# Optimization experiments

Hardware: AMD Instinct MI355X
Metric: run time of the kernel (lower is better)

The kernel has to match this reference:

```python
import jax, jax.numpy as jnp
import numpy as np

D_MODEL = 1024
NUM_MODULES = 8
MAX_TRANSLATION = 3.0
MAX_ROT_ANGLE = 3.141592653589793


def setup_inputs() -> dict:
    key = jax.random.key(0)
    k1, k2, k3, k4 = jax.random.split(key, 4)
    B, N = 8, 8192
    node_feats = jax.random.normal(k1, (B, N, D_MODEL), jnp.float32)
    coords = jax.random.normal(k2, (B, N, 3), jnp.float32)
    W = jax.random.normal(k3, (NUM_MODULES * 8, D_MODEL), jnp.float32) * (1.0 / np.sqrt(D_MODEL))
    b = jax.random.normal(k4, (NUM_MODULES * 8,), jnp.float32) * 0.01
    return {"node_feats": node_feats, "coords": coords, "W": W, "b": b}


def _normalize(x, eps=1e-12):
    return x / jnp.clip(jnp.linalg.norm(x, axis=-1, keepdims=True), eps)


def _axis_angle_to_quaternion(aa):
    # pytorch3d convention: quat = [cos(theta/2), axis * sin(theta/2)]
    angles = jnp.linalg.norm(aa, axis=-1, keepdims=True)
    half = angles * 0.5
    small = jnp.abs(angles) < 1e-6
    safe_angles = jnp.where(small, 1.0, angles)
    sin_half_over_angle = jnp.where(small, 0.5 - angles * angles / 48.0, jnp.sin(half) / safe_angles)
    return jnp.concatenate([jnp.cos(half), aa * sin_half_over_angle], axis=-1)


def _quat_mul(a, b):
    aw, ax, ay, az = a[..., 0], a[..., 1], a[..., 2], a[..., 3]
    bw, bx, by, bz = b[..., 0], b[..., 1], b[..., 2], b[..., 3]
    ow = aw * bw - ax * bx - ay * by - az * bz
    ox = aw * bx + ax * bw + ay * bz - az * by
    oy = aw * by - ax * bz + ay * bw + az * bx
    oz = aw * bz + ax * by - ay * bx + az * bw
    return jnp.stack([ow, ox, oy, oz], axis=-1)


def _quat_apply(q, p):
    # q: [B,1,4], p: [B,N,3] -> rotate points: im(q * (0,p) * q^-1)
    pq = jnp.concatenate([jnp.zeros_like(p[..., :1]), p], axis=-1)
    q_inv = q * jnp.array([1.0, -1.0, -1.0, -1.0], q.dtype)
    return _quat_mul(_quat_mul(q, pq), q_inv)[..., 1:]


def reference(node_feats, coords, W, b):
    B, N, _ = coords.shape
    params = (node_feats @ W.T + b).reshape(B, N, NUM_MODULES, 8)
    anchor_logits = params[..., 0:1]   # [B,N,M,1]
    select_logits = params[..., 1:2]
    rot_axis = params[..., 2:5]
    trans = params[..., 5:8]

    anchor_w = jax.nn.softmax(anchor_logits, axis=1)      # softmax over N
    select_p = jax.nn.sigmoid(select_logits)

    angles = jnp.linalg.norm(rot_axis, axis=-1, keepdims=True)
    axis_n = _normalize(rot_axis)
    angles = jnp.tanh(angles) * MAX_ROT_ANGLE
    quats = _axis_angle_to_quaternion(axis_n * angles)    # [B,N,M,4]
    trans = jnp.tanh(trans) * MAX_TRANSLATION             # [B,N,M,3]

    xs = (jnp.moveaxis(quats, 2, 0),     # [M,B,N,4]
          jnp.moveaxis(trans, 2, 0),     # [M,B,N,3]
          jnp.moveaxis(anchor_w, 2, 0),  # [M,B,N,1]
          jnp.moveaxis(select_p, 2, 0))  # [M,B,N,1]

    def step(c, per):
        q, t, aw, sp = per
        anchor = jnp.sum(c * aw, axis=1, keepdims=True)               # [B,1,3]
        s = jnp.clip(jnp.sum(sp, axis=1, keepdims=True), 1e-8)        # [B,1,1]
        q_group = _normalize(jnp.sum(q * sp, axis=1, keepdims=True) / s)  # [B,1,4]
        t_group = jnp.sum(t * sp, axis=1, keepdims=True) / s          # [B,1,3]
        moved = _quat_apply(q_group, c - anchor) + anchor + t_group   # [B,N,3]
        return c + sp * (moved - c), None                             # lerp

    out, _ = jax.lax.scan(step, coords, xs)
    return out
```

## Files before the change

### kernel.cpp

```cpp
#include <hip/hip_runtime.h>
#include <hip/hip_bf16.h>
#include <hip/hip_fp16.h>
#include <math.h>

#define D_MODEL 1024
#define NMOD 8
#define BATCH 8
#define NNODE 8192
#define PI_F 3.14159265358979323846f
#define MAXT 3.0f

typedef short bf16x8 __attribute__((ext_vector_type(8)));
typedef float f32x4 __attribute__((ext_vector_type(4)));

__device__ inline unsigned short f2bf(float x) {
    __hip_bfloat16 h = __float2bfloat16(x);
    return __builtin_bit_cast(unsigned short, h);
}
__device__ inline float h2f(unsigned short u) {
    __half h = __builtin_bit_cast(__half, u);
    return __half2float(h);
}
__device__ inline unsigned short f2h(float x) {
    __half h = __float2half(x);
    return __builtin_bit_cast(unsigned short, h);
}

__global__ void pack_b(const float* __restrict__ W, unsigned short* __restrict__ Bpk,
                       float* __restrict__ sums) {
    int t = blockIdx.x * 256 + threadIdx.x;
    if (t < BATCH * NMOD * 8) sums[t] = 0.f;
    int l  = t & 63;
    int g  = (t >> 6) & 3;
    int ks = t >> 8;
    int j  = g * 16 + (l & 15);
    int k0 = ks * 32 + ((l >> 4) * 8);
    const float* wp = &W[(size_t)j * D_MODEL + k0];
    bf16x8 pack;
    #pragma unroll
    for (int r = 0; r < 8; ++r) pack[r] = (short)f2bf(wp[r]);
    *reinterpret_cast<bf16x8*>(Bpk + (size_t)t * 8) = pack;
}

__device__ __forceinline__ void loadg2(float4 (&dst)[4], const float* arow, int g) {
    #pragma unroll
    for (int i = 0; i < 2; ++i) {
        dst[2 * i]     = *reinterpret_cast<const float4*>(arow + (g * 2 + i) * 32);
        dst[2 * i + 1] = *reinterpret_cast<const float4*>(arow + (g * 2 + i) * 32 + 4);
    }
}

__device__ __forceinline__ void compg2(const float4 (&src)[4], int g,
                                       const unsigned short* __restrict__ Blds, int lane,
                                       f32x4 (&acc)[4]) {
    #pragma unroll
    for (int i = 0; i < 2; ++i) {
        float f[8] = {src[2*i].x, src[2*i].y, src[2*i].z, src[2*i].w,
                      src[2*i+1].x, src[2*i+1].y, src[2*i+1].z, src[2*i+1].w};
        bf16x8 a;
        #pragma unroll
        for (int j = 0; j < 8; ++j) a[j] = (short)f2bf(f[j]);
        const int ks = g * 2 + i;
        #pragma unroll
        for (int gg = 0; gg < 4; ++gg) {
            bf16x8 bh = *reinterpret_cast<const bf16x8*>(
                Blds + ((size_t)((ks * 4 + gg) * 64 + lane)) * 8);
            acc[gg] = __builtin_amdgcn_mfma_f32_16x16x32_bf16(a, bh, acc[gg], 0, 0, 0);
        }
    }
}

__global__ __launch_bounds__(1024) void gemm_mfma(
    const float* __restrict__ feats, const unsigned short* __restrict__ Bpk,
    const float* __restrict__ bias,
    unsigned int* __restrict__ esp_out,
    float* __restrict__ sums)
{
    __shared__ __align__(16) unsigned char smem[131072];

    const int tid  = threadIdx.x;
    const int lane = tid & 63;
    const int wv   = tid >> 6;

    {
        const char* gsrc = (const char*)Bpk;
        #pragma unroll
        for (int r = 0; r < 8; ++r) {
            const int off = r * 16384 + wv * 1024;
            __builtin_amdgcn_global_load_lds(
                (const __attribute__((address_space(1))) unsigned int*)(gsrc + off + lane * 16),
                (__attribute__((address_space(3))) unsigned int*)(smem + off),
                16, 0, 0);
        }
    }

    const int mt    = blockIdx.x * 16 + wv;
    const int mbase = mt * 16;
    const float* arow = feats + (size_t)(mbase + (lane & 15)) * D_MODEL + ((lane >> 4) * 8);
    const unsigned short* Blds = (const unsigned short*)smem;

    f32x4 acc[4];
    #pragma unroll
    for (int g = 0; g < 4; ++g) acc[g] = (f32x4){0.f, 0.f, 0.f, 0.f};

    float4 Ab[4][4];
    #pragma unroll
    for (int i = 0; i < 4; ++i) loadg2(Ab[i], arow, i);

    __syncthreads();

    #pragma unroll
    for (int i = 0; i < 16; ++i) {
        compg2(Ab[i & 3], i, Blds, lane, acc);
        if (i + 4 < 16) loadg2(Ab[i & 3], arow, i + 4);
    }

    __syncthreads();
    float* pbuf = reinterpret_cast<float*>(smem) + (size_t)wv * (16 * 68);
    float* sacc = reinterpret_cast<float*>(smem + 69632);
    if (tid < 64) sacc[tid] = 0.f;

    #pragma unroll
    for (int g = 0; g < 4; ++g) {
        float bj = bias[g * 16 + (lane & 15)];
        #pragma unroll
        for (int r = 0; r < 4; ++r)
            pbuf[((lane >> 4) * 4 + r) * 68 + g * 16 + (lane & 15)] = acc[g][r] + bj;
    }
    __syncthreads();

    const int b    = mbase >> 13;
    const int nInB = mbase & 8191;

    #pragma unroll
    for (int h = 0; h < 2; ++h) {
        const int node = lane & 15;
        const int m    = (lane >> 4) + 4 * h;
        const float* pa = &pbuf[node * 68 + m * 8];
        float al = pa[0], sl = pa[1];
        float ax = pa[2], ay = pa[3], az = pa[4];
        float tx = pa[5], ty = pa[6], tz = pa[7];

        float ew = expf(al);
        float sp = 1.f / (1.f + expf(-sl));

        float n0  = sqrtf(ax * ax + ay * ay + az * az);
        float inv = 1.f / fmaxf(n0, 1e-12f);
        float ang = tanhf(n0) * PI_F;
        float hf  = 0.5f * ang;
        float shoa = (ang < 1e-6f) ? (0.5f - ang * ang * (1.f / 48.f))
                                   : (sinf(hf) / ang);
        float qw = cosf(hf);
        float fac = inv * ang * shoa;
        float qx = ax * fac, qy = ay * fac, qz = az * fac;

        float ttx = tanhf(tx) * MAXT, tty = tanhf(ty) * MAXT, ttz = tanhf(tz) * MAXT;

        size_t base = ((size_t)(b * NMOD + m)) * NNODE + nInB + node;
        esp_out[base] = ((unsigned)f2h(sp) << 16) | (unsigned)f2h(ew);

        float red[8];
        red[0] = sp;
        red[1] = sp * qw; red[2] = sp * qx; red[3] = sp * qy; red[4] = sp * qz;
        red[5] = sp * ttx; red[6] = sp * tty; red[7] = sp * ttz;
        #pragma unroll
        for (int v = 0; v < 8; ++v) {
            #pragma unroll
            for (int o = 1; o < 16; o <<= 1) red[v] += __shfl_xor(red[v], o);
        }
        if ((lane & 15) == 0) {
            #pragma unroll
            for (int v = 0; v < 8; ++v) atomicAdd(&sacc[m * 8 + v], red[v]);
        }
    }
    __syncthreads();
    if (tid < 64) atomicAdd(&sums[b * 64 + tid], sacc[tid]);
}

__global__ __launch_bounds__(1024) void scan_coords(
    const float* __restrict__ coords,
    const unsigned int* __restrict__ esp_in,
    const float* __restrict__ sums, float* __restrict__ out)
{
    const int b   = blockIdx.x;
    const int tid = threadIdx.x;
    const int lane = tid & 63, wid = tid >> 6;
    __shared__ float redbuf[64];
    __shared__ float bcast[4];

    const int n0 = tid * 8;

    float cx[8], cy[8], cz[8];
    {
        float c[24];
        const float4* cp4 = reinterpret_cast<const float4*>(
            &coords[((size_t)b * NNODE + n0) * 3]);
        #pragma unroll
        for (int q = 0; q < 6; ++q) {
            float4 v = cp4[q];
            c[q * 4 + 0] = v.x; c[q * 4 + 1] = v.y;
            c[q * 4 + 2] = v.z; c[q * 4 + 3] = v.w;
        }
        #pragma unroll
        for (int i = 0; i < 8; ++i) { cx[i] = c[3*i]; cy[i] = c[3*i+1]; cz[i] = c[3*i+2]; }
    }

    const uint4* esp4 = reinterpret_cast<const uint4*>(
        &esp_in[(size_t)b * NMOD * NNODE]);
    uint4 cur0 = esp4[(0 * NNODE + n0) >> 2];
    uint4 cur1 = esp4[((0 * NNODE + n0) >> 2) + 1];

    for (int m = 0; m < NMOD; ++m) {
        const int mn = (m + 1 < NMOD) ? m + 1 : m;
        uint4 nxt0 = esp4[(mn * NNODE + n0) >> 2];
        uint4 nxt1 = esp4[((mn * NNODE + n0) >> 2) + 1];

        unsigned pk[8] = {cur0.x, cur0.y, cur0.z, cur0.w, cur1.x, cur1.y, cur1.z, cur1.w};
        float ev[8], spl[8];
        #pragma unroll
        for (int i = 0; i < 8; ++i) {
            ev[i]  = h2f((unsigned short)(pk[i] & 0xFFFFu));
            spl[i] = h2f((unsigned short)(pk[i] >> 16));
        }

        float se = 0.f, sx = 0.f, sy = 0.f, sz = 0.f;
        #pragma unroll
        for (int i = 0; i < 8; ++i) {
            se += ev[i]; sx += ev[i] * cx[i]; sy += ev[i] * cy[i]; sz += ev[i] * cz[i];
        }
        float vals[4] = {se, sx, sy, sz};
        #pragma unroll
        for (int v = 0; v < 4; ++v) {
            float x = vals[v];
            #pragma unroll
            for (int o = 32; o > 0; o >>= 1) x += __shfl_down(x, o);
            if (lane == 0) redbuf[wid * 4 + v] = x;
        }
        __syncthreads();
        if (wid == 0) {
            float x = redbuf[lane];
            x += __shfl_down(x, 32);
            x += __shfl_down(x, 16);
            x += __shfl_down(x, 8);
            x += __shfl_down(x, 4);
            if (lane < 4) bcast[lane] = x;
        }
        __syncthreads();
        const float SE = bcast[0];
        const float AXc = bcast[1] / SE, AYc = bcast[2] / SE, AZc = bcast[3] / SE;

        const float* sm = &sums[((size_t)b * NMOD + m) * 8];
        float s  = fmaxf(sm[0], 1e-8f);
        float qw = sm[1] / s, qx = sm[2] / s, qy = sm[3] / s, qz = sm[4] / s;
        float qn = sqrtf(qw * qw + qx * qx + qy * qy + qz * qz);
        float qi = 1.f / fmaxf(qn, 1e-12f);
        qw *= qi; qx *= qi; qy *= qi; qz *= qi;

        float xx = qx*qx, yy = qy*qy, zz = qz*qz;
        float xy = qx*qy, xz = qx*qz, yz = qy*qz;
        float wx = qw*qx, wy = qw*qy, wz = qw*qz;
        float r00 = 1.f - 2.f*(yy+zz), r01 = 2.f*(xy-wz),       r02 = 2.f*(xz+wy);
        float r10 = 2.f*(xy+wz),       r11 = 1.f - 2.f*(xx+zz), r12 = 2.f*(yz-wx);
        float r20 = 2.f*(xz-wy),       r21 = 2.f*(yz+wx),       r22 = 1.f - 2.f*(xx+yy);
        float dx = AXc + sm[5] / s, dy = AYc + sm[6] / s, dz = AZc + sm[7] / s;

        #pragma unroll
        for (int i = 0; i < 8; ++i) {
            float px = cx[i] - AXc, py = cy[i] - AYc, pz = cz[i] - AZc;
            float mx = fmaf(r00, px, fmaf(r01, py, fmaf(r02, pz, dx)));
            float my = fmaf(r10, px, fmaf(r11, py, fmaf(r12, pz, dy)));
            float mz = fmaf(r20, px, fmaf(r21, py, fmaf(r22, pz, dz)));
            float sp = spl[i];
            cx[i] = fmaf(sp, mx - cx[i], cx[i]);
            cy[i] = fmaf(sp, my - cy[i], cy[i]);
            cz[i] = fmaf(sp, mz - cz[i], cz[i]);
        }
        cur0 = nxt0; cur1 = nxt1;
        __syncthreads();
    }

    {
        float c[24];
        #pragma unroll
        for (int i = 0; i < 8; ++i) { c[3*i] = cx[i]; c[3*i+1] = cy[i]; c[3*i+2] = cz[i]; }
        float4* op4 = reinterpret_cast<float4*>(&out[((size_t)b * NNODE + n0) * 3]);
        #pragma unroll
        for (int q = 0; q < 6; ++q)
            op4[q] = make_float4(c[q*4+0], c[q*4+1], c[q*4+2], c[q*4+3]);
    }
}

extern "C" void kernel_launch(void* const* d_in, const int* in_sizes, int n_in,
                              void* d_out, int out_size, void* d_ws, size_t ws_size,
                              hipStream_t stream) {
    const float* feats  = (const float*)d_in[0];
    const float* coords = (const float*)d_in[1];
    const float* W      = (const float*)d_in[2];
    const float* bias   = (const float*)d_in[3];
    float* out = (float*)d_out;

    char* ws = (char*)d_ws;
    unsigned short* Bpk = (unsigned short*)(ws);
    unsigned int* esp   = (unsigned int*)(ws + 262144);
    float* sums         = (float*)(ws + 262144 + 2097152);

    pack_b<<<32, 256, 0, stream>>>(W, Bpk, sums);
    gemm_mfma<<<256, 1024, 0, stream>>>(feats, Bpk, bias, esp, sums);
    scan_coords<<<BATCH, 1024, 0, stream>>>(coords, esp, sums, out);
}
```

Before: 91.48 us.

## Fuse GEMM and coordinate scan into one kernel with per-batch completion counters

Merges the GEMM/parameter kernel and the sequential scan kernel into a single launch of 264 blocks. The extra 8 blocks spin on a per-batch atomic counter until all 32 GEMM blocks for that batch have published partial sums. Global float atomics are replaced by per-block partial buffers that the scan block reduces itself. This removes a kernel launch boundary and lets each batch's scan start as soon as its slice of the GEMM is done. The cost is a dependence on the scan blocks being co-resident with or scheduled after the producers, which risks deadlock if scheduling order changes.

```diff
diff --git a/kernel.cpp b/kernel.cpp
--- a/kernel.cpp
+++ b/kernel.cpp
@@ -27,9 +27,9 @@
 }
 
 __global__ void pack_b(const float* __restrict__ W, unsigned short* __restrict__ Bpk,
-                       float* __restrict__ sums) {
+                       int* __restrict__ cnt) {
     int t = blockIdx.x * 256 + threadIdx.x;
-    if (t < BATCH * NMOD * 8) sums[t] = 0.f;
+    if (t < BATCH) cnt[t] = 0;
     int l  = t & 63;
     int g  = (t >> 6) & 3;
     int ks = t >> 8;
@@ -50,243 +50,258 @@
     }
 }
 
-__device__ __forceinline__ void compg2(const float4 (&src)[4], int g,
-                                       const unsigned short* __restrict__ Blds, int lane,
-                                       f32x4 (&acc)[4]) {
-    #pragma unroll
-    for (int i = 0; i < 2; ++i) {
-        float f[8] = {src[2*i].x, src[2*i].y, src[2*i].z, src[2*i].w,
-                      src[2*i+1].x, src[2*i+1].y, src[2*i+1].z, src[2*i+1].w};
-        bf16x8 a;
-        #pragma unroll
-        for (int j = 0; j < 8; ++j) a[j] = (short)f2bf(f[j]);
-        const int ks = g * 2 + i;
-        #pragma unroll
-        for (int gg = 0; gg < 4; ++gg) {
-            bf16x8 bh = *reinterpret_cast<const bf16x8*>(
-                Blds + ((size_t)((ks * 4 + gg) * 64 + lane)) * 8);
-            acc[gg] = __builtin_amdgcn_mfma_f32_16x16x32_bf16(a, bh, acc[gg], 0, 0, 0);
-        }
-    }
-}
-
-__global__ __launch_bounds__(1024) void gemm_mfma(
+__global__ __launch_bounds__(1024) void fused(
     const float* __restrict__ feats, const unsigned short* __restrict__ Bpk,
-    const float* __restrict__ bias,
-    unsigned int* __restrict__ esp_out,
-    float* __restrict__ sums)
+    const float* __restrict__ bias, const float* __restrict__ coords,
+    unsigned int* __restrict__ esp,
+    float* __restrict__ partials,
+    int* __restrict__ cnt,
+    float* __restrict__ out)
 {
     __shared__ __align__(16) unsigned char smem[131072];
-
+    const int bid  = blockIdx.x;
     const int tid  = threadIdx.x;
     const int lane = tid & 63;
     const int wv   = tid >> 6;
 
-    {
-        const char* gsrc = (const char*)Bpk;
-        #pragma unroll
-        for (int r = 0; r < 8; ++r) {
-            const int off = r * 16384 + wv * 1024;
-            __builtin_amdgcn_global_load_lds(
-                (const __attribute__((address_space(1))) unsigned int*)(gsrc + off + lane * 16),
-                (__attribute__((address_space(3))) unsigned int*)(smem + off),
-                16, 0, 0);
-        }
-    }
-
-    const int mt    = blockIdx.x * 16 + wv;
-    const int mbase = mt * 16;
-    const float* arow = feats + (size_t)(mbase + (lane & 15)) * D_MODEL + ((lane >> 4) * 8);
-    const unsigned short* Blds = (const unsigned short*)smem;
-
-    f32x4 acc[4];
-    #pragma unroll
-    for (int g = 0; g < 4; ++g) acc[g] = (f32x4){0.f, 0.f, 0.f, 0.f};
-
-    float4 Ab[4][4];
-    #pragma unroll
-    for (int i = 0; i < 4; ++i) loadg2(Ab[i], arow, i);
-
-    __syncthreads();
-
-    #pragma unroll
-    for (int i = 0; i < 16; ++i) {
-        compg2(Ab[i & 3], i, Blds, lane, acc);
-        if (i + 4 < 16) loadg2(Ab[i & 3], arow, i + 4);
-    }
-
-    __syncthreads();
-    float* pbuf = reinterpret_cast<float*>(smem) + (size_t)wv * (16 * 68);
-    float* sacc = reinterpret_cast<float*>(smem + 69632);
-    if (tid < 64) sacc[tid] = 0.f;
-
-    #pragma unroll
-    for (int g = 0; g < 4; ++g) {
-        float bj = bias[g * 16 + (lane & 15)];
-        #pragma unroll
-        for (int r = 0; r < 4; ++r)
-            pbuf[((lane >> 4) * 4 + r) * 68 + g * 16 + (lane & 15)] = acc[g][r] + bj;
-    }
-    __syncthreads();
-
-    const int b    = mbase >> 13;
-    const int nInB = mbase & 8191;
-
-    #pragma unroll
-    for (int h = 0; h < 2; ++h) {
-        const int node = lane & 15;
-        const int m    = (lane >> 4) + 4 * h;
-        const float* pa = &pbuf[node * 68 + m * 8];
-        float al = pa[0], sl = pa[1];
-        float ax = pa[2], ay = pa[3], az = pa[4];
-        float tx = pa[5], ty = pa[6], tz = pa[7];
-
-        float ew = expf(al);
-        float sp = 1.f / (1.f + expf(-sl));
-
-        float n0  = sqrtf(ax * ax + ay * ay + az * az);
-        float inv = 1.f / fmaxf(n0, 1e-12f);
-        float ang = tanhf(n0) * PI_F;
-        float hf  = 0.5f * ang;
-        float shoa = (ang < 1e-6f) ? (0.5f - ang * ang * (1.f / 48.f))
-                                   : (sinf(hf) / ang);
-        float qw = cosf(hf);
-        float fac = inv * ang * shoa;
-        float qx = ax * fac, qy = ay * fac, qz = az * fac;
-
-        float ttx = tanhf(tx) * MAXT, tty = tanhf(ty) * MAXT, ttz = tanhf(tz) * MAXT;
-
-        size_t base = ((size_t)(b * NMOD + m)) * NNODE + nInB + node;
-        esp_out[base] = ((unsigned)f2h(sp) << 16) | (unsigned)f2h(ew);
-
-        float red[8];
-        red[0] = sp;
-        red[1] = sp * qw; red[2] = sp * qx; red[3] = sp * qy; red[4] = sp * qz;
-        red[5] = sp * ttx; red[6] = sp * tty; red[7] = sp * ttz;
-        #pragma unroll
-        for (int v = 0; v < 8; ++v) {
-            #pragma unroll
-            for (int o = 1; o < 16; o <<= 1) red[v] += __shfl_xor(red[v], o);
-        }
-        if ((lane & 15) == 0) {
-            #pragma unroll
-            for (int v = 0; v < 8; ++v) atomicAdd(&sacc[m * 8 + v], red[v]);
-        }
-    }
-    __syncthreads();
-    if (tid < 64) atomicAdd(&sums[b * 64 + tid], sacc[tid]);
-}
-
-__global__ __launch_bounds__(1024) void scan_coords(
-    const float* __restrict__ coords,
-    const unsigned int* __restrict__ esp_in,
-    const float* __restrict__ sums, float* __restrict__ out)
-{
-    const int b   = blockIdx.x;
-    const int tid = threadIdx.x;
-    const int lane = tid & 63, wid = tid >> 6;
-    __shared__ float redbuf[64];
-    __shared__ float bcast[4];
-
-    const int n0 = tid * 8;
-
-    float cx[8], cy[8], cz[8];
-    {
-        float c[24];
-        const float4* cp4 = reinterpret_cast<const float4*>(
-            &coords[((size_t)b * NNODE + n0) * 3]);
-        #pragma unroll
-        for (int q = 0; q < 6; ++q) {
-            float4 v = cp4[q];
-            c[q * 4 + 0] = v.x; c[q * 4 + 1] = v.y;
-            c[q * 4 + 2] = v.z; c[q * 4 + 3] = v.w;
-        }
-        #pragma unroll
-        for (int i = 0; i < 8; ++i) { cx[i] = c[3*i]; cy[i] = c[3*i+1]; cz[i] = c[3*i+2]; }
-    }
-
-    const uint4* esp4 = reinterpret_cast<const uint4*>(
-        &esp_in[(size_t)b * NMOD * NNODE]);
-    uint4 cur0 = esp4[(0 * NNODE + n0) >> 2];
-    uint4 cur1 = esp4[((0 * NNODE + n0) >> 2) + 1];
-
-    for (int m = 0; m < NMOD; ++m) {
-        const int mn = (m + 1 < NMOD) ? m + 1 : m;
-        uint4 nxt0 = esp4[(mn * NNODE + n0) >> 2];
-        uint4 nxt1 = esp4[((mn * NNODE + n0) >> 2) + 1];
-
-        unsigned pk[8] = {cur0.x, cur0.y, cur0.z, cur0.w, cur1.x, cur1.y, cur1.z, cur1.w};
-        float ev[8], spl[8];
-        #pragma unroll
-        for (int i = 0; i < 8; ++i) {
-            ev[i]  = h2f((unsigned short)(pk[i] & 0xFFFFu));
-            spl[i] = h2f((unsigned short)(pk[i] >> 16));
-        }
-
-        float se = 0.f, sx = 0.f, sy = 0.f, sz = 0.f;
-        #pragma unroll
-        for (int i = 0; i < 8; ++i) {
-            se += ev[i]; sx += ev[i] * cx[i]; sy += ev[i] * cy[i]; sz += ev[i] * cz[i];
-        }
-        float vals[4] = {se, sx, sy, sz};
-        #pragma unroll
-        for (int v = 0; v < 4; ++v) {
-            float x = vals[v];
-            #pragma unroll
-            for (int o = 32; o > 0; o >>= 1) x += __shfl_down(x, o);
-            if (lane == 0) redbuf[wid * 4 + v] = x;
-        }
-        __syncthreads();
-        if (wid == 0) {
-            float x = redbuf[lane];
-            x += __shfl_down(x, 32);
-            x += __shfl_down(x, 16);
-            x += __shfl_down(x, 8);
-            x += __shfl_down(x, 4);
-            if (lane < 4) bcast[lane] = x;
-        }
-        __syncthreads();
-        const float SE = bcast[0];
-        const float AXc = bcast[1] / SE, AYc = bcast[2] / SE, AZc = bcast[3] / SE;
-
-        const float* sm = &sums[((size_t)b * NMOD + m) * 8];
-        float s  = fmaxf(sm[0], 1e-8f);
-        float qw = sm[1] / s, qx = sm[2] / s, qy = sm[3] / s, qz = sm[4] / s;
-        float qn = sqrtf(qw * qw + qx * qx + qy * qy + qz * qz);
-        float qi = 1.f / fmaxf(qn, 1e-12f);
-        qw *= qi; qx *= qi; qy *= qi; qz *= qi;
-
-        float xx = qx*qx, yy = qy*qy, zz = qz*qz;
-        float xy = qx*qy, xz = qx*qz, yz = qy*qz;
-        float wx = qw*qx, wy = qw*qy, wz = qw*qz;
-        float r00 = 1.f - 2.f*(yy+zz), r01 = 2.f*(xy-wz),       r02 = 2.f*(xz+wy);
-        float r10 = 2.f*(xy+wz),       r11 = 1.f - 2.f*(xx+zz), r12 = 2.f*(yz-wx);
-        float r20 = 2.f*(xz-wy),       r21 = 2.f*(yz+wx),       r22 = 1.f - 2.f*(xx+yy);
-        float dx = AXc + sm[5] / s, dy = AYc + sm[6] / s, dz = AZc + sm[7] / s;
-
-        #pragma unroll
-        for (int i = 0; i < 8; ++i) {
-            float px = cx[i] - AXc, py = cy[i] - AYc, pz = cz[i] - AZc;
-            float mx = fmaf(r00, px, fmaf(r01, py, fmaf(r02, pz, dx)));
-            float my = fmaf(r10, px, fmaf(r11, py, fmaf(r12, pz, dy)));
-            float mz = fmaf(r20, px, fmaf(r21, py, fmaf(r22, pz, dz)));
-            float sp = spl[i];
-            cx[i] = fmaf(sp, mx - cx[i], cx[i]);
-            cy[i] = fmaf(sp, my - cy[i], cy[i]);
-            cz[i] = fmaf(sp, mz - cz[i], cz[i]);
-        }
-        cur0 = nxt0; cur1 = nxt1;
-        __syncthreads();
-    }
-
-    {
-        float c[24];
-        #pragma unroll
-        for (int i = 0; i < 8; ++i) { c[3*i] = cx[i]; c[3*i+1] = cy[i]; c[3*i+2] = cz[i]; }
-        float4* op4 = reinterpret_cast<float4*>(&out[((size_t)b * NNODE + n0) * 3]);
-        #pragma unroll
-        for (int q = 0; q < 6; ++q)
-            op4[q] = make_float4(c[q*4+0], c[q*4+1], c[q*4+2], c[q*4+3]);
+    if (bid < 256) {
+        {
+            const char* gsrc = (const char*)Bpk;
+            #pragma unroll
+            for (int r = 0; r < 8; ++r) {
+                const int off = r * 16384 + wv * 1024;
+                __builtin_amdgcn_global_load_lds(
+                    (const __attribute__((address_space(1))) unsigned int*)(gsrc + off + lane * 16),
+                    (__attribute__((address_space(3))) unsigned int*)(smem + off),
+                    16, 0, 0);
+            }
+        }
+
+        const int mt    = bid * 16 + wv;
+        const int mbase = mt * 16;
+        const float* arow = feats + (size_t)(mbase + (lane & 15)) * D_MODEL + ((lane >> 4) * 8);
+        const unsigned short* Blds = (const unsigned short*)smem;
+
+        f32x4 acc[4];
+        #pragma unroll
+        for (int g = 0; g < 4; ++g) acc[g] = (f32x4){0.f, 0.f, 0.f, 0.f};
+
+        float4 Ab[4][4];
+        #pragma unroll
+        for (int i = 0; i < 4; ++i) loadg2(Ab[i], arow, i);
+
+        __syncthreads();
+
+        #pragma unroll
+        for (int i = 0; i < 16; ++i) {
+            {
+                const float4 (&src)[4] = Ab[i & 3];
+                #pragma unroll
+                for (int ii = 0; ii < 2; ++ii) {
+                    float f[8] = {src[2*ii].x, src[2*ii].y, src[2*ii].z, src[2*ii].w,
+                                  src[2*ii+1].x, src[2*ii+1].y, src[2*ii+1].z, src[2*ii+1].w};
+                    bf16x8 a;
+                    #pragma unroll
+                    for (int j = 0; j < 8; ++j) a[j] = (short)f2bf(f[j]);
+                    const int ks = i * 2 + ii;
+                    #pragma unroll
+                    for (int gg = 0; gg < 4; ++gg) {
+                        bf16x8 bh = *reinterpret_cast<const bf16x8*>(
+                            Blds + ((size_t)((ks * 4 + gg) * 64 + lane)) * 8);
+                        acc[gg] = __builtin_amdgcn_mfma_f32_16x16x32_bf16(a, bh, acc[gg], 0, 0, 0);
+                    }
+                }
+            }
+            if (i + 4 < 16) loadg2(Ab[i & 3], arow, i + 4);
+        }
+
+        __syncthreads();
+        float* pbuf = reinterpret_cast<float*>(smem) + (size_t)wv * (16 * 68);
+        float* sacc = reinterpret_cast<float*>(smem + 69632);
+        if (tid < 64) sacc[tid] = 0.f;
+
+        #pragma unroll
+        for (int g = 0; g < 4; ++g) {
+            float bj = bias[g * 16 + (lane & 15)];
+            #pragma unroll
+            for (int r = 0; r < 4; ++r)
+                pbuf[((lane >> 4) * 4 + r) * 68 + g * 16 + (lane & 15)] = acc[g][r] + bj;
+        }
+        __syncthreads();
+
+        const int b    = mbase >> 13;
+        const int nInB = mbase & 8191;
+
+        #pragma unroll
+        for (int h = 0; h < 2; ++h) {
+            const int node = lane & 15;
+            const int m    = (lane >> 4) + 4 * h;
+            const float* pa = &pbuf[node * 68 + m * 8];
+            float al = pa[0], sl = pa[1];
+            float ax = pa[2], ay = pa[3], az = pa[4];
+            float tx = pa[5], ty = pa[6], tz = pa[7];
+
+            float ew = expf(al);
+            float sp = 1.f / (1.f + expf(-sl));
+
+            float n0  = sqrtf(ax * ax + ay * ay + az * az);
+            float inv = 1.f / fmaxf(n0, 1e-12f);
+            float ang = tanhf(n0) * PI_F;
+            float hf  = 0.5f * ang;
+            float shoa = (ang < 1e-6f) ? (0.5f - ang * ang * (1.f / 48.f))
+                                       : (sinf(hf) / ang);
+            float qw = cosf(hf);
+            float fac = inv * ang * shoa;
+            float qx = ax * fac, qy = ay * fac, qz = az * fac;
+
+            float ttx = tanhf(tx) * MAXT, tty = tanhf(ty) * MAXT, ttz = tanhf(tz) * MAXT;
+
+            size_t base = ((size_t)(b * NMOD + m)) * NNODE + nInB + node;
+            esp[base] = ((unsigned)f2h(sp) << 16) | (unsigned)f2h(ew);
+
+            float red[8];
+            red[0] = sp;
+            red[1] = sp * qw; red[2] = sp * qx; red[3] = sp * qy; red[4] = sp * qz;
+            red[5] = sp * ttx; red[6] = sp * tty; red[7] = sp * ttz;
+            #pragma unroll
+            for (int v = 0; v < 8; ++v) {
+                #pragma unroll
+                for (int o = 1; o < 16; o <<= 1) red[v] += __shfl_xor(red[v], o);
+            }
+            if ((lane & 15) == 0) {
+                #pragma unroll
+                for (int v = 0; v < 8; ++v) atomicAdd(&sacc[m * 8 + v], red[v]);
+            }
+        }
+        __syncthreads();
+
+        if (tid < 64) {
+            partials[((size_t)b * 32 + (bid & 31)) * 64 + tid] = sacc[tid];
+            __threadfence();
+            if (tid == 0)
+                __hip_atomic_fetch_add(&cnt[b], 1, __ATOMIC_RELEASE, __HIP_MEMORY_SCOPE_AGENT);
+        }
+    } else {
+        const int b = bid - 256;
+        float* redbuf = reinterpret_cast<float*>(smem);
+        float* bcast  = reinterpret_cast<float*>(smem) + 64;
+        float* smod   = reinterpret_cast<float*>(smem) + 96;
+
+        const int n0 = tid * 8;
+        const int wid = wv;
+
+        float cx[8], cy[8], cz[8];
+        {
+            float c[24];
+            const float4* cp4 = reinterpret_cast<const float4*>(
+                &coords[((size_t)b * NNODE + n0) * 3]);
+            #pragma unroll
+            for (int q = 0; q < 6; ++q) {
+                float4 v = cp4[q];
+                c[q * 4 + 0] = v.x; c[q * 4 + 1] = v.y;
+                c[q * 4 + 2] = v.z; c[q * 4 + 3] = v.w;
+            }
+            #pragma unroll
+            for (int i = 0; i < 8; ++i) { cx[i] = c[3*i]; cy[i] = c[3*i+1]; cz[i] = c[3*i+2]; }
+        }
+
+        if (tid == 0) {
+            while (__hip_atomic_load(&cnt[b], __ATOMIC_ACQUIRE, __HIP_MEMORY_SCOPE_AGENT) < 32)
+                __builtin_amdgcn_s_sleep(8);
+        }
+        __syncthreads();
+
+        if (tid < 64) {
+            float s = 0.f;
+            #pragma unroll 4
+            for (int blk = 0; blk < 32; ++blk)
+                s += partials[((size_t)b * 32 + blk) * 64 + tid];
+            smod[tid] = s;
+        }
+        __syncthreads();
+
+        const uint4* esp4 = reinterpret_cast<const uint4*>(&esp[(size_t)b * NMOD * NNODE]);
+        uint4 cur0 = esp4[(0 * NNODE + n0) >> 2];
+        uint4 cur1 = esp4[((0 * NNODE + n0) >> 2) + 1];
+
+        for (int m = 0; m < NMOD; ++m) {
+            const int mn = (m + 1 < NMOD) ? m + 1 : m;
+            uint4 nxt0 = esp4[(mn * NNODE + n0) >> 2];
+            uint4 nxt1 = esp4[((mn * NNODE + n0) >> 2) + 1];
+
+            unsigned pk[8] = {cur0.x, cur0.y, cur0.z, cur0.w, cur1.x, cur1.y, cur1.z, cur1.w};
+            float ev[8], spl[8];
+            #pragma unroll
+            for (int i = 0; i < 8; ++i) {
+                ev[i]  = h2f((unsigned short)(pk[i] & 0xFFFFu));
+                spl[i] = h2f((unsigned short)(pk[i] >> 16));
+            }
+
+            float se = 0.f, sx = 0.f, sy = 0.f, sz = 0.f;
+            #pragma unroll
+            for (int i = 0; i < 8; ++i) {
+                se += ev[i]; sx += ev[i] * cx[i]; sy += ev[i] * cy[i]; sz += ev[i] * cz[i];
+            }
+            float vals[4] = {se, sx, sy, sz};
+            #pragma unroll
+            for (int v = 0; v < 4; ++v) {
+                float x = vals[v];
+                #pragma unroll
+                for (int o = 32; o > 0; o >>= 1) x += __shfl_down(x, o);
+                if (lane == 0) redbuf[wid * 4 + v] = x;
+            }
+            __syncthreads();
+            if (wid == 0) {
+                float x = redbuf[lane];
+                x += __shfl_down(x, 32);
+                x += __shfl_down(x, 16);
+                x += __shfl_down(x, 8);
+                x += __shfl_down(x, 4);
+                if (lane < 4) bcast[lane] = x;
+            }
+            __syncthreads();
+            const float SE = bcast[0];
+            const float AXc = bcast[1] / SE, AYc = bcast[2] / SE, AZc = bcast[3] / SE;
+
+            const float* sm = &smod[m * 8];
+            float s  = fmaxf(sm[0], 1e-8f);
+            float qw = sm[1] / s, qx = sm[2] / s, qy = sm[3] / s, qz = sm[4] / s;
+            float qn = sqrtf(qw * qw + qx * qx + qy * qy + qz * qz);
+            float qi = 1.f / fmaxf(qn, 1e-12f);
+            qw *= qi; qx *= qi; qy *= qi; qz *= qi;
+
+            float xx = qx*qx, yy = qy*qy, zz = qz*qz;
+            float xy = qx*qy, xz = qx*qz, yz = qy*qz;
+            float wx = qw*qx, wy = qw*qy, wz = qw*qz;
+            float r00 = 1.f - 2.f*(yy+zz), r01 = 2.f*(xy-wz),       r02 = 2.f*(xz+wy);
+            float r10 = 2.f*(xy+wz),       r11 = 1.f - 2.f*(xx+zz), r12 = 2.f*(yz-wx);
+            float r20 = 2.f*(xz-wy),       r21 = 2.f*(yz+wx),       r22 = 1.f - 2.f*(xx+yy);
+            float dx = AXc + sm[5] / s, dy = AYc + sm[6] / s, dz = AZc + sm[7] / s;
+
+            #pragma unroll
+            for (int i = 0; i < 8; ++i) {
+                float px = cx[i] - AXc, py = cy[i] - AYc, pz = cz[i] - AZc;
+                float mx = fmaf(r00, px, fmaf(r01, py, fmaf(r02, pz, dx)));
+                float my = fmaf(r10, px, fmaf(r11, py, fmaf(r12, pz, dy)));
+                float mz = fmaf(r20, px, fmaf(r21, py, fmaf(r22, pz, dz)));
+                float sp = spl[i];
+                cx[i] = fmaf(sp, mx - cx[i], cx[i]);
+                cy[i] = fmaf(sp, my - cy[i], cy[i]);
+                cz[i] = fmaf(sp, mz - cz[i], cz[i]);
+            }
+            cur0 = nxt0; cur1 = nxt1;
+            __syncthreads();
+        }
+
+        {
+            float c[24];
+            #pragma unroll
+            for (int i = 0; i < 8; ++i) { c[3*i] = cx[i]; c[3*i+1] = cy[i]; c[3*i+2] = cz[i]; }
+            float4* op4 = reinterpret_cast<float4*>(&out[((size_t)b * NNODE + n0) * 3]);
+            #pragma unroll
+            for (int q = 0; q < 6; ++q)
+                op4[q] = make_float4(c[q*4+0], c[q*4+1], c[q*4+2], c[q*4+3]);
+        }
     }
 }
 
@@ -302,9 +317,9 @@
     char* ws = (char*)d_ws;
     unsigned short* Bpk = (unsigned short*)(ws);
     unsigned int* esp   = (unsigned int*)(ws + 262144);
-    float* sums         = (float*)(ws + 262144 + 2097152);
-
-    pack_b<<<32, 256, 0, stream>>>(W, Bpk, sums);
-    gemm_mfma<<<256, 1024, 0, stream>>>(feats, Bpk, bias, esp, sums);
-    scan_coords<<<BATCH, 1024, 0, stream>>>(coords, esp, sums, out);
-}
+    float* partials     = (float*)(ws + 262144 + 2097152);
+    int* cnt            = (int*)(ws + 262144 + 2097152 + 65536);
+
+    pack_b<<<32, 256, 0, stream>>>(W, Bpk, cnt);
+    fused<<<264, 1024, 0, stream>>>(feats, Bpk, bias, coords, esp, partials, cnt, out);
+}
```

After: 96.02 us. +5.0%, slower.
